# Kernel optimization log

Measured on AMD Instinct MI355X. Metric: run time of the kernel, lower is better.

## Reference

```python
import jax, jax.numpy as jnp
import numpy as np

N = 50000          # num nodes
E = 800000         # num edges (before self loops)
F = 128            # input feature dim
UNITS = 128        # output units
ATT_UNITS = 128    # attention units (Q/K dim)
HEADS = 8


def setup_inputs() -> dict:
    key = jax.random.key(0)
    ks = jax.random.split(key, 6)
    s = 1.0 / np.sqrt(F).astype(np.float32)  # ~glorot scale
    return {
        "x": jax.random.normal(ks[0], (N, F), dtype=jnp.float32),
        "edge_index": jax.random.randint(ks[1], (2, E), 0, N, dtype=jnp.int32),
        "query_kernel": jax.random.normal(ks[2], (F, ATT_UNITS), dtype=jnp.float32) * s,
        "query_bias": jnp.zeros((ATT_UNITS,), jnp.float32),
        "key_kernel": jax.random.normal(ks[3], (F, ATT_UNITS), dtype=jnp.float32) * s,
        "key_bias": jnp.zeros((ATT_UNITS,), jnp.float32),
        "kernel": jax.random.normal(ks[4], (F, UNITS), dtype=jnp.float32) * s,
        "bias": jnp.zeros((UNITS,), jnp.float32),
    }


def segment_softmax(scores, seg, num_segments):
    # scores: [E', H], seg: [E'] -> softmax over edges sharing the same target node, per head
    smax = jax.ops.segment_max(scores, seg, num_segments=num_segments)
    sexp = jnp.exp(scores - smax[seg])
    ssum = jax.ops.segment_sum(sexp, seg, num_segments=num_segments)
    return sexp / ssum[seg]


def reference(x, edge_index, query_kernel, query_bias, key_kernel, key_bias, kernel, bias):
    num_nodes = x.shape[0]
    # add self-loop edges (as in tf_geometric add_self_loop_edge)
    loop = jnp.arange(num_nodes, dtype=edge_index.dtype)
    row = jnp.concatenate([edge_index[0], loop])  # target nodes, [E']
    col = jnp.concatenate([edge_index[1], loop])  # source nodes, [E']

    Q = jax.nn.relu(x @ query_kernel + query_bias)[row]  # [E', A]
    K = jax.nn.relu(x @ key_kernel + key_bias)[col]      # [E', A]
    V = (x @ kernel)[col]                                 # [E', U]

    # split into attention heads: tf.split(..., num_heads, axis=-1)
    Qh = Q.reshape(-1, HEADS, ATT_UNITS // HEADS)
    Kh = K.reshape(-1, HEADS, ATT_UNITS // HEADS)
    att = jnp.sum(Qh * Kh, axis=-1)                       # [E', H]
    alpha = segment_softmax(att, row, num_nodes)          # [E', H]

    # split_value_heads=True: split V into head slices, weight, scatter-add, concat
    Vh = V.reshape(-1, HEADS, UNITS // HEADS)             # [E', H, U/H]
    msg = Vh * alpha[:, :, None]
    out = jax.ops.segment_sum(msg, row, num_segments=num_nodes)  # [N, H, U/H]
    out = out.reshape(num_nodes, UNITS)
    out = out + bias  # use_bias=True, activation=None
    return out
```

## Files before the change

### kernel.cpp

```cpp
#include <hip/hip_runtime.h>
#include <hip/hip_fp16.h>
#include <cstdint>

#define FDIM 128
#define XSTR 136
#define NROWTILE 128
#define WCHUNKS ((FDIM * XSTR * 2) / 1024)
#define XCHUNKS ((NROWTILE * XSTR * 2) / 1024)
#define CSRS 128

typedef __attribute__((ext_vector_type(8))) _Float16 half8;
typedef __attribute__((ext_vector_type(2))) _Float16 h2;
typedef __attribute__((ext_vector_type(16))) float float16;

#if defined(__has_builtin)
#if __has_builtin(__builtin_amdgcn_fdot2)
#define HAVE_FDOT2 1
#endif
#endif

__device__ __forceinline__ void gload_lds16(const void* g, void* s) {
    __builtin_amdgcn_global_load_lds(
        (const __attribute__((address_space(1))) void*)g,
        (__attribute__((address_space(3))) void*)s, 16, 0, 0);
}

__device__ __forceinline__ h2 as_h2(unsigned u) {
    union { unsigned u; h2 h; } c; c.u = u; return c.h;
}
__device__ __forceinline__ float2 h2_to_f2(unsigned u) {
    __half2 h = *(__half2*)&u;
    return __half22float2(h);
}

__global__ __launch_bounds__(256) void edges_k(
    const float* __restrict__ x, __half* __restrict__ XH,
    const int* __restrict__ ei, int E,
    const float* __restrict__ Wq, const float* __restrict__ Wk,
    const float* __restrict__ Wv, __half* __restrict__ WTH,
    int* __restrict__ deg, int* __restrict__ csr, int N, int Npad)
{
    int idx = blockIdx.x * 256 + threadIdx.x;

    if (idx < Npad * 32) {
        int row = idx >> 5;
        int c = (idx & 31) << 2;
        float4 v = make_float4(0.f, 0.f, 0.f, 0.f);
        if (row < N) v = *(const float4*)(x + (size_t)row * FDIM + c);
        __half h[4] = {__float2half_rn(v.x), __float2half_rn(v.y),
                       __float2half_rn(v.z), __float2half_rn(v.w)};
        *(ushort4*)(XH + (size_t)row * XSTR + c) = *(ushort4*)h;
    }

    if (idx < 3 * FDIM * FDIM) {
        int mat = idx >> 14;
        int m = idx & 16383;
        int k = m >> 7;
        int nn = m & 127;
        const float* __restrict__ W = (mat == 0) ? Wq : (mat == 1) ? Wk : Wv;
        WTH[(size_t)mat * FDIM * XSTR + nn * XSTR + k] =
            __float2half_rn(W[k * FDIM + nn]);
    }

    if (idx < E) {
        int row = ei[idx];
        int col = ei[E + idx];
        int slot = atomicAdd(&deg[row], 1);
        if (slot < CSRS) csr[(row << 7) + slot] = col;
    }
}

__global__ __launch_bounds__(256) void gemm_mfma_k(
    const __half* __restrict__ XH, const __half* __restrict__ WTH,
    const float* __restrict__ bq, const float* __restrict__ bk,
    const float* __restrict__ bias,
    __half* __restrict__ Qb, uint2* __restrict__ KV, int N)
{
    __shared__ __half xs[NROWTILE * XSTR];
    __shared__ __half ws[FDIM * XSTR];

    const int tid  = threadIdx.x;
    const int wave = tid >> 6;
    const int lane = tid & 63;
    const int r0   = blockIdx.x * NROWTILE;
    const int mat  = blockIdx.y;

    const char* wbase = (const char*)(WTH + (size_t)mat * FDIM * XSTR);
    for (int c = wave; c < XCHUNKS; c += 4) {
        gload_lds16((const char*)(XH + (size_t)r0 * XSTR) + c * 1024 + lane * 16,
                    (char*)xs + c * 1024);
        gload_lds16(wbase + c * 1024 + lane * 16, (char*)ws + c * 1024);
    }
    __syncthreads();

    const int mrow = lane & 31;
    const int half = lane >> 5;
    const int arow = wave * 32 + mrow;

    float16 acc[4];
    #pragma unroll
    for (int nt = 0; nt < 4; ++nt)
        #pragma unroll
        for (int r = 0; r < 16; ++r) acc[nt][r] = 0.f;

    #pragma unroll
    for (int ks = 0; ks < 8; ++ks) {
        const int ko = ks * 16 + half * 8;
        half8 ah = *(const half8*)(xs + arow * XSTR + ko);
        #pragma unroll
        for (int nt = 0; nt < 4; ++nt) {
            half8 bh = *(const half8*)(ws + (nt * 32 + mrow) * XSTR + ko);
            acc[nt] = __builtin_amdgcn_mfma_f32_32x32x16_f16(ah, bh, acc[nt], 0, 0, 0);
        }
    }

    __syncthreads();

    const float* bvec = (mat == 0) ? bq : (mat == 1) ? bk : bias;
    #pragma unroll
    for (int nt = 0; nt < 4; ++nt) {
        const int col = nt * 32 + mrow;
        const float bb = bvec[col];
        #pragma unroll
        for (int reg = 0; reg < 16; ++reg) {
            int rl = wave * 32 + (reg & 3) + 8 * (reg >> 2) + 4 * half;
            float v = acc[nt][reg] + bb;
            if (mat < 2) v = fmaxf(v, 0.f);
            ws[rl * XSTR + col] = __float2half_rn(v);
        }
    }
    __syncthreads();

    if (mat == 0) {
        #pragma unroll
        for (int it = 0; it < 8; ++it) {
            int idx = it * 256 + tid;
            int row = idx >> 4;
            int c = (idx & 15) * 8;
            uint4 v = *(const uint4*)(ws + row * XSTR + c);
            if (r0 + row < N)
                *(uint4*)(Qb + (size_t)(r0 + row) * FDIM + c) = v;
        }
    } else {
        __half* kvh = (__half*)KV;
        const int sub = (mat == 2) ? 2 : 0;
        #pragma unroll
        for (int it = 0; it < 32; ++it) {
            int idx = it * 256 + tid;
            int row = idx >> 6;
            int p = idx & 63;
            unsigned v = *(const unsigned*)(ws + row * XSTR + 2 * p);
            if (r0 + row < N)
                *(unsigned*)(kvh + (size_t)(r0 + row) * 256 + p * 4 + sub) = v;
        }
    }
}

__global__ __launch_bounds__(256) void aggregate_k(
    const __half* __restrict__ Qb, const uint2* __restrict__ KV,
    const int* __restrict__ deg, const int* __restrict__ csr,
    float* __restrict__ out, int N)
{
    const int lane = threadIdx.x & 63;
    int n = blockIdx.x * 4 + (threadIdx.x >> 6);
    if (n >= N) return;
    n = __builtin_amdgcn_readfirstlane(n);

    int d = __builtin_amdgcn_readfirstlane(deg[n]);
    if (d > CSRS) d = CSRS;
    const int off   = n << 7;
    const int total = d + 1;

    const unsigned qu = *(const unsigned*)(Qb + (size_t)n * FDIM + 2 * lane);
    const h2 q2 = as_h2(qu);
    const float2 qf = h2_to_f2(qu);
    (void)qf; (void)q2;

    float acc0 = 0.f, acc1 = 0.f, lsum = 0.f;

    auto proc = [&](uint2 kv) {
#ifdef HAVE_FDOT2
        float p = __builtin_amdgcn_fdot2(as_h2(kv.x), q2, 0.0f, false);
#else
        float2 kf = h2_to_f2(kv.x);
        float p = qf.x * kf.x + qf.y * kf.y;
#endif
        p += __shfl_xor(p, 1);
        p += __shfl_xor(p, 2);
        p += __shfl_xor(p, 4);
        float s = __expf(p);
        float2 vf = h2_to_f2(kv.y);
        lsum += s;
        acc0 += s * vf.x;
        acc1 += s * vf.y;
    };

    int idxbuf[8];
    #pragma unroll
    for (int u = 0; u < 8; ++u)
        idxbuf[u] = (u == 0) ? n : ((u < total) ? csr[off + u - 1] : 0);

    int t = 0;
    while (t + 8 <= total) {
        uint2 kv[8];
        #pragma unroll
        for (int u = 0; u < 8; ++u)
            kv[u] = KV[(((unsigned)idxbuf[u]) << 6) + lane];
        #pragma unroll
        for (int u = 0; u < 8; ++u) {
            int nx = t + 8 + u;
            idxbuf[u] = (nx < total) ? csr[off + nx - 1] : 0;
        }
        #pragma unroll
        for (int u = 0; u < 8; ++u) proc(kv[u]);
        t += 8;
    }
    for (; t < total; ++t) {
        int c = (t == 0) ? n : csr[off + t - 1];
        uint2 kv = KV[(((unsigned)c) << 6) + lane];
        proc(kv);
    }

    const float inv = 1.0f / lsum;
    float2 o;
    o.x = acc0 * inv;
    o.y = acc1 * inv;
    *(float2*)(out + (size_t)n * FDIM + 2 * lane) = o;
}

extern "C" void kernel_launch(void* const* d_in, const int* in_sizes, int n_in,
                              void* d_out, int out_size, void* d_ws, size_t ws_size,
                              hipStream_t stream)
{
    const float* x    = (const float*)d_in[0];
    const int*   ei   = (const int*)d_in[1];
    const float* Wq   = (const float*)d_in[2];
    const float* bq   = (const float*)d_in[3];
    const float* Wk   = (const float*)d_in[4];
    const float* bk   = (const float*)d_in[5];
    const float* Wv   = (const float*)d_in[6];
    const float* bias = (const float*)d_in[7];
    float* out = (float*)d_out;

    const int N = in_sizes[0] / FDIM;
    const int E = in_sizes[1] / 2;
    const int nblk = (N + NROWTILE - 1) / NROWTILE;
    const int Npad = nblk * NROWTILE;

    __half* WTH = (__half*)d_ws;
    __half* XH  = WTH + (size_t)3 * FDIM * XSTR;
    __half* Qb  = XH + (size_t)Npad * XSTR;
    uint2*  KV  = (uint2*)(Qb + (size_t)N * FDIM);
    int* deg    = (int*)(KV + (size_t)N * 64);
    int* csr    = deg + N;

    (void)hipMemsetAsync(deg, 0, (size_t)N * sizeof(int), stream);

    edges_k<<<(Npad * 32 + 255) / 256, 256, 0, stream>>>(
        x, XH, ei, E, Wq, Wk, Wv, WTH, deg, csr, N, Npad);

    gemm_mfma_k<<<dim3(nblk, 3), 256, 0, stream>>>(
        XH, WTH, bq, bk, bias, Qb, KV, N);

    aggregate_k<<<(N + 3) / 4, 256, 0, stream>>>(Qb, KV, deg, csr, out, N);
}
```

Baseline: 210.3 us.

## Make aggregate kernel persistent with prefetch of next node's metadata

The aggregation kernel now runs a fixed grid of 2048 blocks, and each wave strides over nodes. While a wave processes the current node, it prefetches the next node's degree, query slice and first eight CSR indices, so that latency is hidden across nodes. The scalar tail loop is replaced by padded 8-wide batches in which inactive slots are masked to zero weight. This cuts launch and tail costs and overlaps index loads, but it uses more registers per wave and does wasted gathers of node 0 for the padded slots.

```diff
diff --git a/kernel.cpp b/kernel.cpp
--- a/kernel.cpp
+++ b/kernel.cpp
@@ -159,73 +159,89 @@
 __global__ __launch_bounds__(256) void aggregate_k(
     const __half* __restrict__ Qb, const uint2* __restrict__ KV,
     const int* __restrict__ deg, const int* __restrict__ csr,
-    float* __restrict__ out, int N)
+    float* __restrict__ out, int N, int nwaves)
 {
     const int lane = threadIdx.x & 63;
-    int n = blockIdx.x * 4 + (threadIdx.x >> 6);
-    if (n >= N) return;
-    n = __builtin_amdgcn_readfirstlane(n);
-
-    int d = __builtin_amdgcn_readfirstlane(deg[n]);
-    if (d > CSRS) d = CSRS;
-    const int off   = n << 7;
-    const int total = d + 1;
-
-    const unsigned qu = *(const unsigned*)(Qb + (size_t)n * FDIM + 2 * lane);
-    const h2 q2 = as_h2(qu);
-    const float2 qf = h2_to_f2(qu);
-    (void)qf; (void)q2;
-
-    float acc0 = 0.f, acc1 = 0.f, lsum = 0.f;
-
-    auto proc = [&](uint2 kv) {
+    int wid = __builtin_amdgcn_readfirstlane(blockIdx.x * 4 + (threadIdx.x >> 6));
+    if (wid >= N) return;
+
+    int n0 = wid;
+    int d0 = deg[n0];
+    unsigned qu0 = *(const unsigned*)(Qb + (size_t)n0 * FDIM + 2 * lane);
+    int idx0[8];
+    idx0[0] = n0;
+    #pragma unroll
+    for (int u = 1; u < 8; ++u) idx0[u] = csr[(n0 << 7) + u - 1];
+
+    for (;;) {
+        const int n1 = n0 + nwaves;
+        const bool has1 = (n1 < N);
+        int d1 = 0;
+        unsigned qu1 = 0;
+        int idx1[8];
+        #pragma unroll
+        for (int u = 0; u < 8; ++u) idx1[u] = 0;
+        if (has1) {
+            d1 = deg[n1];
+            qu1 = *(const unsigned*)(Qb + (size_t)n1 * FDIM + 2 * lane);
+            idx1[0] = n1;
+            #pragma unroll
+            for (int u = 1; u < 8; ++u) idx1[u] = csr[(n1 << 7) + u - 1];
+        }
+
+        const int d = (d0 > CSRS) ? CSRS : d0;
+        const int total = d + 1;
+        const int off = n0 << 7;
+        const h2 q2 = as_h2(qu0);
+#ifndef HAVE_FDOT2
+        const float2 qf = h2_to_f2(qu0);
+#endif
+        float acc0 = 0.f, acc1 = 0.f, lsum = 0.f;
+
+        #pragma unroll
+        for (int u = 1; u < 8; ++u)
+            if (u >= total) idx0[u] = 0;
+
+        for (int t = 0; t < total; t += 8) {
+            uint2 kv[8];
+            #pragma unroll
+            for (int u = 0; u < 8; ++u)
+                kv[u] = KV[(((unsigned)idx0[u]) << 6) + lane];
+            #pragma unroll
+            for (int u = 0; u < 8; ++u) {
+                int nx = t + 8 + u;
+                idx0[u] = (nx < total) ? csr[off + nx - 1] : 0;
+            }
+            #pragma unroll
+            for (int u = 0; u < 8; ++u) {
 #ifdef HAVE_FDOT2
-        float p = __builtin_amdgcn_fdot2(as_h2(kv.x), q2, 0.0f, false);
+                float p = __builtin_amdgcn_fdot2(as_h2(kv[u].x), q2, 0.0f, false);
 #else
-        float2 kf = h2_to_f2(kv.x);
-        float p = qf.x * kf.x + qf.y * kf.y;
-#endif
-        p += __shfl_xor(p, 1);
-        p += __shfl_xor(p, 2);
-        p += __shfl_xor(p, 4);
-        float s = __expf(p);
-        float2 vf = h2_to_f2(kv.y);
-        lsum += s;
-        acc0 += s * vf.x;
-        acc1 += s * vf.y;
-    };
-
-    int idxbuf[8];
-    #pragma unroll
-    for (int u = 0; u < 8; ++u)
-        idxbuf[u] = (u == 0) ? n : ((u < total) ? csr[off + u - 1] : 0);
-
-    int t = 0;
-    while (t + 8 <= total) {
-        uint2 kv[8];
-        #pragma unroll
-        for (int u = 0; u < 8; ++u)
-            kv[u] = KV[(((unsigned)idxbuf[u]) << 6) + lane];
-        #pragma unroll
-        for (int u = 0; u < 8; ++u) {
-            int nx = t + 8 + u;
-            idxbuf[u] = (nx < total) ? csr[off + nx - 1] : 0;
-        }
-        #pragma unroll
-        for (int u = 0; u < 8; ++u) proc(kv[u]);
-        t += 8;
-    }
-    for (; t < total; ++t) {
-        int c = (t == 0) ? n : csr[off + t - 1];
-        uint2 kv = KV[(((unsigned)c) << 6) + lane];
-        proc(kv);
-    }
-
-    const float inv = 1.0f / lsum;
-    float2 o;
-    o.x = acc0 * inv;
-    o.y = acc1 * inv;
-    *(float2*)(out + (size_t)n * FDIM + 2 * lane) = o;
+                float2 kf = h2_to_f2(kv[u].x);
+                float p = qf.x * kf.x + qf.y * kf.y;
+#endif
+                p += __shfl_xor(p, 1);
+                p += __shfl_xor(p, 2);
+                p += __shfl_xor(p, 4);
+                float s = (t + u < total) ? __expf(p) : 0.f;
+                float2 vf = h2_to_f2(kv[u].y);
+                lsum += s;
+                acc0 += s * vf.x;
+                acc1 += s * vf.y;
+            }
+        }
+
+        const float inv = 1.0f / lsum;
+        float2 o;
+        o.x = acc0 * inv;
+        o.y = acc1 * inv;
+        *(float2*)(out + (size_t)n0 * FDIM + 2 * lane) = o;
+
+        if (!has1) break;
+        n0 = n1; d0 = d1; qu0 = qu1;
+        #pragma unroll
+        for (int u = 0; u < 8; ++u) idx0[u] = idx1[u];
+    }
 }
 
 extern "C" void kernel_launch(void* const* d_in, const int* in_sizes, int n_in,
@@ -262,5 +278,7 @@
     gemm_mfma_k<<<dim3(nblk, 3), 256, 0, stream>>>(
         XH, WTH, bq, bk, bias, Qb, KV, N);
 
-    aggregate_k<<<(N + 3) / 4, 256, 0, stream>>>(Qb, KV, deg, csr, out, N);
-}
+    int ablk = 2048;
+    if (ablk * 4 > N) ablk = (N + 3) / 4;
+    aggregate_k<<<ablk, 256, 0, stream>>>(Qb, KV, deg, csr, out, N, ablk * 4);
+}
```

After: 215.3 us. 1.02x slower.
